# Kernel tuning notes

Measured on AMD Instinct MI355X. Metric: run time of the kernel, lower is better.

The kernel has to match this reference:

```python
import jax, jax.numpy as jnp
import numpy as np

B, S, D, F, E, DT, K = 4, 2048, 1024, 4096, 8, 256, 2


def setup_inputs() -> dict:
    key = jax.random.key(0)
    ks = jax.random.split(key, 8)
    scale_g = 1.0 / np.sqrt(D)
    scale_t = 1.0 / np.sqrt(DT)
    scale_1 = 1.0 / np.sqrt(D)
    scale_2 = 1.0 / np.sqrt(F)
    return {
        "inputs": jax.random.normal(ks[0], (B, S, D), dtype=jnp.float32),
        "task_param": jax.random.normal(ks[1], (B, 1, DT), dtype=jnp.float32),
        "Wg_in": jax.random.normal(ks[2], (D, E), dtype=jnp.float32) * scale_g,
        "bg_in": jnp.zeros((E,), dtype=jnp.float32),
        "Wg_task": jax.random.normal(ks[3], (DT, E), dtype=jnp.float32) * scale_t,
        "bg_task": jnp.zeros((E,), dtype=jnp.float32),
        "alpha": jnp.float32(0.5),
        "W1": jax.random.normal(ks[4], (E, D, F), dtype=jnp.float32) * scale_1,
        "b1": jnp.zeros((E, F), dtype=jnp.float32),
        "W2": jax.random.normal(ks[5], (E, F, D), dtype=jnp.float32) * scale_2,
        "b2": jnp.zeros((E, D), dtype=jnp.float32),
    }


def reference(inputs, task_param, Wg_in, bg_in, Wg_task, bg_task, alpha, W1, b1, W2, b2):
    # Gating: blend input-gate and task-gate logits ([B,1,E] broadcasts over S)
    input_logits = jnp.einsum('bsd,de->bse', inputs, Wg_in) + bg_in
    task_logits = jnp.einsum('btd,de->bte', task_param, Wg_task) + bg_task
    gate_logits = (1.0 - alpha) * input_logits + alpha * task_logits  # [B,S,E]

    topk_vals, selected = jax.lax.top_k(gate_logits, K)  # [B,S,K]

    # Load-balancing auxiliary loss (float32 softmax, as in the original)
    weights_softmax = jax.nn.softmax(gate_logits.astype(jnp.float32), axis=-1).astype(inputs.dtype)
    average_weight = jnp.mean(weights_softmax, axis=(0, 1))  # [E]
    onehot = jax.nn.one_hot(selected, E, dtype=inputs.dtype)  # [B,S,K,E]
    average_count = jnp.mean(onehot.sum(axis=2), axis=(0, 1))  # [E]
    l_aux = jnp.mean(average_weight * average_count) * E

    # Combine weights: softmax over the top-k gate values
    w = jax.nn.softmax(topk_vals.astype(jnp.float32), axis=-1).astype(inputs.dtype)  # [B,S,K]

    # Dense expert compute (same math as the per-expert gather/scatter loop)
    h = jax.nn.silu(jnp.einsum('bsd,edf->ebsf', inputs, W1) + b1[:, None, None, :])  # [E,B,S,F]
    expert_out = jnp.einsum('ebsf,efd->ebsd', h, W2) + b2[:, None, None, :]          # [E,B,S,D]

    picked = jnp.einsum('bske,ebsd->bskd', onehot, expert_out)  # [B,S,K,D]
    results = jnp.einsum('bsk,bskd->bsd', w, picked)            # [B,S,D]
    return results, l_aux.astype(jnp.float32)
```

## Files before the change

### kernel.cpp

```cpp
#include <hip/hip_runtime.h>

#define T_TOK 8192
#define D_DIM 1024
#define F_DIM 4096
#define E_EXP 8
#define DT_DIM 256
#define GBLK 256

#define A_XB   0u
#define A_WT   16777216u
#define A_H    83886080u
#define A_Y    226492416u
#define A_META 262144000u
#define MO_FILL   0
#define MO_PB     64
#define MO_NT     128
#define MO_PARTP  256
#define MO_PARTC  8448
#define MO_TILEE  16640
#define MO_TILERB 17664
#define MO_ROUTEE 18688
#define MO_ROUTEW 84224
#define MO_TSLOT  149760
#define MO_PTOK   215296
#define META_BYTES 284928
#define META_INTS  (META_BYTES/4)

using bf16x8 = __attribute__((ext_vector_type(8))) short;
using f32x4  = __attribute__((ext_vector_type(4))) float;
typedef unsigned short u16;

__device__ __forceinline__ u16 f2bf(float f) {
  union { float f; unsigned u; } v; v.f = f;
  unsigned r = v.u + 0x7FFFu + ((v.u >> 16) & 1u);
  return (u16)(r >> 16);
}
__device__ __forceinline__ float bf2f(u16 h) {
  union { unsigned u; float f; } v; v.u = ((unsigned)h) << 16; return v.f;
}
__device__ __forceinline__ void gload16(const void* gsrc, void* ldst) {
  __builtin_amdgcn_global_load_lds(
      (const __attribute__((address_space(1))) void*)gsrc,
      (__attribute__((address_space(3))) void*)ldst, 16, 0, 0);
}

__global__ void zerok(int* p, int n) {
  int i = blockIdx.x * 256 + threadIdx.x;
  if (i < n) p[i] = 0;
}

__global__ __launch_bounds__(256) void tcvt(const float* __restrict__ src,
                                            u16* __restrict__ dst, int R, int C) {
  __shared__ u16 tile[32][33];
  size_t off = (size_t)blockIdx.z * R * C;
  int cb = blockIdx.x * 32, rb = blockIdx.y * 32;
  int tx = threadIdx.x & 31, ty = threadIdx.x >> 5;
#pragma unroll
  for (int i = 0; i < 4; i++)
    tile[ty + i * 8][tx] = f2bf(src[off + (size_t)(rb + ty + i * 8) * C + cb + tx]);
  __syncthreads();
#pragma unroll
  for (int i = 0; i < 4; i++)
    dst[off + (size_t)(cb + ty + i * 8) * R + rb + tx] = tile[tx][ty + i * 8];
}

__global__ __launch_bounds__(256) void gating(
    const float* __restrict__ X, const float* __restrict__ TP,
    const float* __restrict__ Wg, const float* __restrict__ bg,
    const float* __restrict__ Wt, const float* __restrict__ bgt,
    const float* __restrict__ alphaP, u16* __restrict__ Xb, int* meta) {
  __shared__ float WgT[E_EXP * D_DIM];
  __shared__ float WtT[E_EXP * DT_DIM];
  __shared__ float wsP[4][8];
  __shared__ int   wsC[4][8];
  int tid = threadIdx.x;
  for (int i = tid; i < E_EXP * D_DIM; i += 256) { int d = i >> 3, e = i & 7; WgT[e * D_DIM + d] = Wg[i]; }
  for (int i = tid; i < E_EXP * DT_DIM; i += 256) { int d = i >> 3, e = i & 7; WtT[e * DT_DIM + d] = Wt[i]; }
  __syncthreads();
  int lane = tid & 63, wid = tid >> 6;
  int tb = blockIdx.x * 32;
  int b = tb >> 11;
  float alpha = alphaP[0];

  float tac[8] = {};
#pragma unroll
  for (int i = 0; i < 4; i++) {
    int d = lane + i * 64;
    float x = TP[b * DT_DIM + d];
#pragma unroll
    for (int e = 0; e < 8; e++) tac[e] += x * WtT[e * DT_DIM + d];
  }
  for (int off = 32; off > 0; off >>= 1)
#pragma unroll
    for (int e = 0; e < 8; e++) tac[e] += __shfl_xor(tac[e], off);
  float tl[8];
#pragma unroll
  for (int e = 0; e < 8; e++) tl[e] = alpha * (tac[e] + bgt[e]);

  float psum[8] = {};
  int   cnt[8] = {};
  for (int i = 0; i < 8; i++) {
    int t = tb + wid * 8 + i;
    const float* xr = X + (size_t)t * D_DIM;
    float acc[8] = {};
    u16 xb[16];
#pragma unroll 4
    for (int j = 0; j < 16; j++) {
      int d = lane + j * 64;
      float x = xr[d];
      xb[j] = f2bf(x);
#pragma unroll
      for (int e = 0; e < 8; e++) acc[e] += x * WgT[e * D_DIM + d];
    }
#pragma unroll
    for (int j = 0; j < 16; j++) Xb[(size_t)t * D_DIM + lane + j * 64] = xb[j];
    for (int off = 32; off > 0; off >>= 1)
#pragma unroll
      for (int e = 0; e < 8; e++) acc[e] += __shfl_xor(acc[e], off);
    float gl[8];
#pragma unroll
    for (int e = 0; e < 8; e++) gl[e] = (1.f - alpha) * (acc[e] + bg[e]) + tl[e];
    int e1 = 0;
#pragma unroll
    for (int e = 1; e < 8; e++) if (gl[e] > gl[e1]) e1 = e;
    int es = (e1 == 0) ? 1 : 0;
#pragma unroll
    for (int e = 0; e < 8; e++) if (e != e1 && gl[e] > gl[es]) es = e;
    float mx = gl[0];
#pragma unroll
    for (int e = 1; e < 8; e++) mx = fmaxf(mx, gl[e]);
    float pe[8], se = 0.f;
#pragma unroll
    for (int e = 0; e < 8; e++) { pe[e] = __expf(gl[e] - mx); se += pe[e]; }
    float inv = 1.f / se;
    if (lane == 0) {
#pragma unroll
      for (int e = 0; e < 8; e++) psum[e] += pe[e] * inv;
      cnt[e1]++; cnt[es]++;
      float w1 = 1.f / (1.f + __expf(gl[es] - gl[e1]));
      meta[MO_ROUTEE / 4 + 2 * t] = e1;
      meta[MO_ROUTEE / 4 + 2 * t + 1] = es;
      ((float*)meta)[MO_ROUTEW / 4 + 2 * t] = w1;
      ((float*)meta)[MO_ROUTEW / 4 + 2 * t + 1] = 1.f - w1;
    }
  }
  if (lane == 0) {
#pragma unroll
    for (int e = 0; e < 8; e++) { wsP[wid][e] = psum[e]; wsC[wid][e] = cnt[e]; }
  }
  __syncthreads();
  if (tid < 8) {
    float p = wsP[0][tid] + wsP[1][tid] + wsP[2][tid] + wsP[3][tid];
    int   c = wsC[0][tid] + wsC[1][tid] + wsC[2][tid] + wsC[3][tid];
    ((float*)meta)[MO_PARTP / 4 + blockIdx.x * 8 + tid] = p;
    meta[MO_PARTC / 4 + blockIdx.x * 8 + tid] = c;
  }
}

__global__ void plan(int* meta, float* out) {
  __shared__ float sp[8];
  __shared__ int   sc[8];
  int tid = threadIdx.x;
  if (blockIdx.x != 0) return;
  if (tid < 8) {
    const float* pp = (const float*)meta + MO_PARTP / 4;
    const int*   pc = meta + MO_PARTC / 4;
    float p = 0.f; int c = 0;
    for (int b = 0; b < GBLK; b++) { p += pp[b * 8 + tid]; c += pc[b * 8 + tid]; }
    sp[tid] = p; sc[tid] = c;
  }
  __syncthreads();
  if (tid == 0) {
    int* pb = meta + MO_PB / 4;
    int* tileE = meta + MO_TILEE / 4;
    int* tileRB = meta + MO_TILERB / 4;
    int base = 0, nt = 0;
    float la = 0.f;
    for (int e = 0; e < 8; e++) {
      int n = sc[e];
      pb[e] = base;
      int ntl = (n + 127) >> 7;
      for (int i = 0; i < ntl; i++) { tileE[nt] = e; tileRB[nt] = base + (i << 7); nt++; }
      base += ntl << 7;
      la += (sp[e] * (1.f / 8192.f)) * ((float)n * (1.f / 8192.f));
    }
    pb[8] = base;
    meta[MO_NT / 4] = nt;
    out[T_TOK * D_DIM] = la;
  }
}

__global__ __launch_bounds__(256) void fillk(int* meta) {
  int t = blockIdx.x * 256 + threadIdx.x;
  int lane = threadIdx.x & 63;
  int* pb = meta + MO_PB / 4;
  int* fl = meta + MO_FILL / 4;
  int* ptok = meta + MO_PTOK / 4;
  int* ts = meta + MO_TSLOT / 4;
  unsigned long long lmask = (1ull << lane) - 1;
#pragma unroll
  for (int k = 0; k < 2; k++) {
    int e = meta[MO_ROUTEE / 4 + 2 * t + k];
    int slot = 0;
    for (int ee = 0; ee < 8; ee++) {
      unsigned long long mask = __ballot(e == ee);
      if (e == ee) {
        int low = __ffsll((long long)mask) - 1;
        int pre = __popcll(mask & lmask);
        int base = 0;
        if (lane == low) base = atomicAdd(&fl[ee], __popcll(mask));
        base = __shfl(base, low);
        slot = pb[ee] + base + pre;
      }
    }
    ptok[slot] = t;
    ts[2 * t + k] = slot;
  }
}


__global__ __launch_bounds__(256) void gemm1(
    const u16* __restrict__ Xb, const u16* __restrict__ W1T,
    const float* __restrict__ b1, u16* __restrict__ H, const int* __restrict__ meta) {
  int xcd = blockIdx.x & 7, loc = blockIdx.x >> 3;
  int bt = loc >> 2;
  int cb = (xcd * 4 + (loc & 3)) * 128;
  int nt = meta[MO_NT / 4];
  if (bt >= nt) return;
  int e = meta[MO_TILEE / 4 + bt];
  int rb = meta[MO_TILERB / 4 + bt];
  const int* ptok = meta + MO_PTOK / 4;

  __shared__ short sA[2][128 * 32];
  __shared__ short sB[2][128 * 32];
  int tid = threadIdx.x, lane = tid & 63, wid = tid >> 6;
  int wr = wid >> 1, wc = wid & 1;
  int r0 = tid >> 2;
  int c0 = (((tid & 3) ^ ((r0 >> 1) & 3)) << 3);
  int tok0 = ptok[rb + r0];
  int tok1 = ptok[rb + r0 + 64];
  const u16* gA0 = Xb + (size_t)tok0 * D_DIM + c0;
  const u16* gA1 = Xb + (size_t)tok1 * D_DIM + c0;
  const u16* gB0 = W1T + ((size_t)e * F_DIM + cb + r0) * D_DIM + c0;
  const u16* gB1 = gB0 + (size_t)64 * D_DIM;

#define STAGE_G1(buf, k0)                                              \
  {                                                                    \
    gload16(gA0 + (k0), (char*)&sA[buf][0] + wid * 1024);              \
    gload16(gA1 + (k0), (char*)&sA[buf][0] + 4096 + wid * 1024);       \
    gload16(gB0 + (k0), (char*)&sB[buf][0] + wid * 1024);              \
    gload16(gB1 + (k0), (char*)&sB[buf][0] + 4096 + wid * 1024);       \
  }

  f32x4 acc[4][4] = {};
  int kb = (((lane >> 4) ^ (((lane & 15) >> 1) & 3)) << 3);
  int ra = wr * 64 + (lane & 15);
  int rn = wc * 64 + (lane & 15);
  STAGE_G1(0, 0)
  for (int k0 = 0; k0 < D_DIM; k0 += 32) {
    int c = (k0 >> 5) & 1;
    asm volatile("s_waitcnt vmcnt(0) lgkmcnt(0)" ::: "memory");
    __builtin_amdgcn_sched_barrier(0);
    __builtin_amdgcn_s_barrier();
    if (k0 + 32 < D_DIM) STAGE_G1(c ^ 1, k0 + 32)
    const short* pA = &sA[c][0];
    const short* pB = &sB[c][0];
    bf16x8 af[4], bfr[4];
#pragma unroll
    for (int m = 0; m < 4; m++)
      af[m] = *(const bf16x8*)((const char*)pA + ((ra + m * 16) * 32 + kb) * 2);
#pragma unroll
    for (int n = 0; n < 4; n++)
      bfr[n] = *(const bf16x8*)((const char*)pB + ((rn + n * 16) * 32 + kb) * 2);
    __builtin_amdgcn_s_setprio(1);
#pragma unroll
    for (int m = 0; m < 4; m++)
#pragma unroll
      for (int n = 0; n < 4; n++)
        acc[m][n] = __builtin_amdgcn_mfma_f32_16x16x32_bf16(af[m], bfr[n], acc[m][n], 0, 0, 0);
    __builtin_amdgcn_s_setprio(0);
  }
  int rbase = wr * 64 + ((lane >> 4) << 2);
  int cbase = cb + wc * 64 + (lane & 15);
#pragma unroll
  for (int m = 0; m < 4; m++)
#pragma unroll
    for (int n = 0; n < 4; n++) {
      int f = cbase + n * 16;
      float bias = b1[e * F_DIM + f];
#pragma unroll
      for (int r = 0; r < 4; r++) {
        int p = rb + rbase + m * 16 + r;
        float v = acc[m][n][r] + bias;
        float s = v * (1.0f / (1.0f + __expf(-v)));
        H[(size_t)p * F_DIM + f] = f2bf(s);
      }
    }
}

__global__ __launch_bounds__(256) void gemm2(
    const u16* __restrict__ H, const u16* __restrict__ W2T,
    const float* __restrict__ b2, u16* __restrict__ Y, const int* __restrict__ meta) {
  int id = blockIdx.x;
  int wg = (id & 7) * 136 + (id >> 3);
  int bt = wg >> 3;
  int cb = (wg & 7) * 128;
  int nt = meta[MO_NT / 4];
  if (bt >= nt) return;
  int e = meta[MO_TILEE / 4 + bt];
  int rb = meta[MO_TILERB / 4 + bt];
  __shared__ short sA[2][128 * 32];
  __shared__ short sB[2][128 * 32];
  int tid = threadIdx.x, lane = tid & 63, wid = tid >> 6;
  int wr = wid >> 1, wc = wid & 1;
  int r0 = tid >> 2;
  int c0 = (((tid & 3) ^ ((r0 >> 1) & 3)) << 3);
  const u16* gA0 = H + (size_t)(rb + r0) * F_DIM + c0;
  const u16* gA1 = gA0 + (size_t)64 * F_DIM;
  const u16* gB0 = W2T + ((size_t)e * D_DIM + cb + r0) * F_DIM + c0;
  const u16* gB1 = gB0 + (size_t)64 * F_DIM;

#define STAGE_G2(buf, k0)                                              \
  {                                                                    \
    gload16(gA0 + (k0), (char*)&sA[buf][0] + wid * 1024);              \
    gload16(gA1 + (k0), (char*)&sA[buf][0] + 4096 + wid * 1024);       \
    gload16(gB0 + (k0), (char*)&sB[buf][0] + wid * 1024);              \
    gload16(gB1 + (k0), (char*)&sB[buf][0] + 4096 + wid * 1024);       \
  }

  f32x4 acc[4][4] = {};
  int kb = (((lane >> 4) ^ (((lane & 15) >> 1) & 3)) << 3);
  int ra = wr * 64 + (lane & 15);
  int rn = wc * 64 + (lane & 15);
  STAGE_G2(0, 0)
  for (int k0 = 0; k0 < F_DIM; k0 += 32) {
    int c = (k0 >> 5) & 1;
    asm volatile("s_waitcnt vmcnt(0) lgkmcnt(0)" ::: "memory");
    __builtin_amdgcn_sched_barrier(0);
    __builtin_amdgcn_s_barrier();
    if (k0 + 32 < F_DIM) STAGE_G2(c ^ 1, k0 + 32)
    const short* pA = &sA[c][0];
    const short* pB = &sB[c][0];
    bf16x8 af[4], bfr[4];
#pragma unroll
    for (int m = 0; m < 4; m++)
      af[m] = *(const bf16x8*)((const char*)pA + ((ra + m * 16) * 32 + kb) * 2);
#pragma unroll
    for (int n = 0; n < 4; n++)
      bfr[n] = *(const bf16x8*)((const char*)pB + ((rn + n * 16) * 32 + kb) * 2);
    __builtin_amdgcn_s_setprio(1);
#pragma unroll
    for (int m = 0; m < 4; m++)
#pragma unroll
      for (int n = 0; n < 4; n++)
        acc[m][n] = __builtin_amdgcn_mfma_f32_16x16x32_bf16(af[m], bfr[n], acc[m][n], 0, 0, 0);
    __builtin_amdgcn_s_setprio(0);
  }
  int rbase = wr * 64 + ((lane >> 4) << 2);
  int cbase = cb + wc * 64 + (lane & 15);
#pragma unroll
  for (int m = 0; m < 4; m++)
#pragma unroll
    for (int n = 0; n < 4; n++) {
      int d = cbase + n * 16;
      float bias = b2[e * D_DIM + d];
#pragma unroll
      for (int r = 0; r < 4; r++) {
        int p = rb + rbase + m * 16 + r;
        Y[(size_t)p * D_DIM + d] = f2bf(acc[m][n][r] + bias);
      }
    }
}

__global__ __launch_bounds__(256) void combine(const u16* __restrict__ Y,
                                               const int* __restrict__ meta,
                                               float* __restrict__ out) {
  int t = blockIdx.x;
  const int* ts = meta + MO_TSLOT / 4;
  const float* rw = (const float*)meta + MO_ROUTEW / 4;
  int s1 = ts[2 * t], s2 = ts[2 * t + 1];
  float w1 = rw[2 * t], w2 = rw[2 * t + 1];
  int d0 = threadIdx.x * 4;
  ushort4 a = *(const ushort4*)(Y + (size_t)s1 * D_DIM + d0);
  ushort4 b = *(const ushort4*)(Y + (size_t)s2 * D_DIM + d0);
  float4 v;
  v.x = w1 * bf2f(a.x) + w2 * bf2f(b.x);
  v.y = w1 * bf2f(a.y) + w2 * bf2f(b.y);
  v.z = w1 * bf2f(a.z) + w2 * bf2f(b.z);
  v.w = w1 * bf2f(a.w) + w2 * bf2f(b.w);
  *(float4*)(out + (size_t)t * D_DIM + d0) = v;
}

extern "C" void kernel_launch(void* const* d_in, const int* in_sizes, int n_in,
                              void* d_out, int out_size, void* d_ws, size_t ws_size,
                              hipStream_t stream) {
  (void)in_sizes; (void)n_in; (void)out_size; (void)ws_size;
  const float* X    = (const float*)d_in[0];
  const float* TP   = (const float*)d_in[1];
  const float* Wg   = (const float*)d_in[2];
  const float* bg   = (const float*)d_in[3];
  const float* Wt   = (const float*)d_in[4];
  const float* bgt  = (const float*)d_in[5];
  const float* alp  = (const float*)d_in[6];
  const float* W1   = (const float*)d_in[7];
  const float* b1   = (const float*)d_in[8];
  const float* W2   = (const float*)d_in[9];
  const float* b2   = (const float*)d_in[10];
  float* out = (float*)d_out;
  char* ws = (char*)d_ws;
  u16* Xb = (u16*)(ws + A_XB);
  u16* WT = (u16*)(ws + A_WT);
  u16* H  = (u16*)(ws + A_H);
  u16* Y  = (u16*)(ws + A_Y);
  int* meta = (int*)(ws + A_META);

  zerok<<<(META_INTS + 255) / 256, 256, 0, stream>>>(meta, META_INTS);
  tcvt<<<dim3(F_DIM / 32, D_DIM / 32, E_EXP), 256, 0, stream>>>(W1, WT, D_DIM, F_DIM);
  gating<<<GBLK, 256, 0, stream>>>(X, TP, Wg, bg, Wt, bgt, alp, Xb, meta);
  plan<<<1, 64, 0, stream>>>(meta, out);
  fillk<<<T_TOK / 256, 256, 0, stream>>>(meta);
  gemm1<<<4352, 256, 0, stream>>>(Xb, WT, b1, H, meta);
  tcvt<<<dim3(D_DIM / 32, F_DIM / 32, E_EXP), 256, 0, stream>>>(W2, WT, F_DIM, D_DIM);
  gemm2<<<1088, 256, 0, stream>>>(H, WT, b2, Y, meta);
  combine<<<T_TOK, 256, 0, stream>>>(Y, meta, out);
}
```

Measured before the change: 588.2 us.

## Fuse gating with W1/W2 bf16 transposes into one prep kernel, drop zero kernel

```diff
diff --git a/kernel.cpp b/kernel.cpp
--- a/kernel.cpp
+++ b/kernel.cpp
@@ -12,6 +12,8 @@
 #define A_H    83886080u
 #define A_Y    226492416u
 #define A_META 262144000u
+#define A_W2T  262428928u
+#define W2T_NEED (262428928ull + 67108864ull)
 #define MO_FILL   0
 #define MO_PB     64
 #define MO_NT     128
@@ -24,7 +26,6 @@
 #define MO_TSLOT  149760
 #define MO_PTOK   215296
 #define META_BYTES 284928
-#define META_INTS  (META_BYTES/4)
 
 using bf16x8 = __attribute__((ext_vector_type(8))) short;
 using f32x4  = __attribute__((ext_vector_type(4))) float;
@@ -44,41 +45,66 @@
       (__attribute__((address_space(3))) void*)ldst, 16, 0, 0);
 }
 
-__global__ void zerok(int* p, int n) {
-  int i = blockIdx.x * 256 + threadIdx.x;
-  if (i < n) p[i] = 0;
-}
-
-__global__ __launch_bounds__(256) void tcvt(const float* __restrict__ src,
-                                            u16* __restrict__ dst, int R, int C) {
-  __shared__ u16 tile[32][33];
-  size_t off = (size_t)blockIdx.z * R * C;
-  int cb = blockIdx.x * 32, rb = blockIdx.y * 32;
-  int tx = threadIdx.x & 31, ty = threadIdx.x >> 5;
-#pragma unroll
-  for (int i = 0; i < 4; i++)
-    tile[ty + i * 8][tx] = f2bf(src[off + (size_t)(rb + ty + i * 8) * C + cb + tx]);
+__device__ __forceinline__ void tcvt64_body(const float* __restrict__ src,
+                                            u16* __restrict__ dst, int R, int C,
+                                            int e, int rb, int cb, char* smem) {
+  u16 (*tile)[65] = (u16(*)[65])smem;
+  size_t off = (size_t)e * R * C;
+  int t = threadIdx.x;
+  int r = t >> 4, cq = (t & 15) << 2;
+#pragma unroll
+  for (int k = 0; k < 4; k++) {
+    int rr = r + k * 16;
+    float4 v = *(const float4*)(src + off + (size_t)(rb + rr) * C + cb + cq);
+    tile[rr][cq] = f2bf(v.x);
+    tile[rr][cq + 1] = f2bf(v.y);
+    tile[rr][cq + 2] = f2bf(v.z);
+    tile[rr][cq + 3] = f2bf(v.w);
+  }
   __syncthreads();
-#pragma unroll
-  for (int i = 0; i < 4; i++)
-    dst[off + (size_t)(cb + ty + i * 8) * R + rb + tx] = tile[tx][ty + i * 8];
-}
-
-__global__ __launch_bounds__(256) void gating(
+  int r4 = (t & 15) << 2, c0 = t >> 4;
+#pragma unroll
+  for (int j = 0; j < 4; j++) {
+    int c = c0 + j * 16;
+    ushort4 o;
+    o.x = tile[r4][c]; o.y = tile[r4 + 1][c];
+    o.z = tile[r4 + 2][c]; o.w = tile[r4 + 3][c];
+    *(ushort4*)(dst + off + (size_t)(cb + c) * R + rb + r4) = o;
+  }
+}
+
+__global__ __launch_bounds__(256) void prep(
     const float* __restrict__ X, const float* __restrict__ TP,
     const float* __restrict__ Wg, const float* __restrict__ bg,
     const float* __restrict__ Wt, const float* __restrict__ bgt,
-    const float* __restrict__ alphaP, u16* __restrict__ Xb, int* meta) {
-  __shared__ float WgT[E_EXP * D_DIM];
-  __shared__ float WtT[E_EXP * DT_DIM];
-  __shared__ float wsP[4][8];
-  __shared__ int   wsC[4][8];
+    const float* __restrict__ alphaP,
+    const float* __restrict__ W1, const float* __restrict__ W2,
+    u16* __restrict__ Xb, u16* __restrict__ W1T, u16* __restrict__ W2T,
+    int* meta) {
+  __shared__ char smem[41216];
+  int bid = blockIdx.x;
+  if (bid >= GBLK) {
+    int loc = bid - GBLK;
+    if (loc < 8192) {
+      int e = loc >> 10, t10 = loc & 1023;
+      tcvt64_body(W1, W1T, D_DIM, F_DIM, e, (t10 & 15) << 6, (t10 >> 4) << 6, smem);
+    } else {
+      int l2 = loc - 8192;
+      int e = l2 >> 10, t10 = l2 & 1023;
+      tcvt64_body(W2, W2T, F_DIM, D_DIM, e, (t10 >> 4) << 6, (t10 & 15) << 6, smem);
+    }
+    return;
+  }
+  float* WgT = (float*)smem;
+  float* WtT = (float*)(smem + 32768);
+  float* wsP = (float*)(smem + 40960);
+  int*   wsC = (int*)(smem + 41088);
   int tid = threadIdx.x;
   for (int i = tid; i < E_EXP * D_DIM; i += 256) { int d = i >> 3, e = i & 7; WgT[e * D_DIM + d] = Wg[i]; }
   for (int i = tid; i < E_EXP * DT_DIM; i += 256) { int d = i >> 3, e = i & 7; WtT[e * DT_DIM + d] = Wt[i]; }
   __syncthreads();
   int lane = tid & 63, wid = tid >> 6;
-  int tb = blockIdx.x * 32;
+  int tb = bid * 32;
   int b = tb >> 11;
   float alpha = alphaP[0];
 
@@ -146,15 +172,23 @@
   }
   if (lane == 0) {
 #pragma unroll
-    for (int e = 0; e < 8; e++) { wsP[wid][e] = psum[e]; wsC[wid][e] = cnt[e]; }
+    for (int e = 0; e < 8; e++) { wsP[wid * 8 + e] = psum[e]; wsC[wid * 8 + e] = cnt[e]; }
   }
   __syncthreads();
   if (tid < 8) {
-    float p = wsP[0][tid] + wsP[1][tid] + wsP[2][tid] + wsP[3][tid];
-    int   c = wsC[0][tid] + wsC[1][tid] + wsC[2][tid] + wsC[3][tid];
-    ((float*)meta)[MO_PARTP / 4 + blockIdx.x * 8 + tid] = p;
-    meta[MO_PARTC / 4 + blockIdx.x * 8 + tid] = c;
-  }
+    float p = wsP[tid] + wsP[8 + tid] + wsP[16 + tid] + wsP[24 + tid];
+    int   c = wsC[tid] + wsC[8 + tid] + wsC[16 + tid] + wsC[24 + tid];
+    ((float*)meta)[MO_PARTP / 4 + bid * 8 + tid] = p;
+    meta[MO_PARTC / 4 + bid * 8 + tid] = c;
+  }
+}
+
+__global__ __launch_bounds__(256) void tcvt2k(const float* __restrict__ W2,
+                                              u16* __restrict__ W2T) {
+  __shared__ char smem[8448];
+  int loc = blockIdx.x;
+  int e = loc >> 10, t10 = loc & 1023;
+  tcvt64_body(W2, W2T, F_DIM, D_DIM, e, (t10 >> 4) << 6, (t10 & 15) << 6, smem);
 }
 
 __global__ void plan(int* meta, float* out) {
@@ -168,7 +202,10 @@
     float p = 0.f; int c = 0;
     for (int b = 0; b < GBLK; b++) { p += pp[b * 8 + tid]; c += pc[b * 8 + tid]; }
     sp[tid] = p; sc[tid] = c;
-  }
+    meta[MO_FILL / 4 + tid] = 0;
+  }
+  int* ptok = meta + MO_PTOK / 4;
+  for (int i = tid; i < 17408; i += 64) ptok[i] = 0;
   __syncthreads();
   if (tid == 0) {
     int* pb = meta + MO_PB / 4;
@@ -394,7 +431,7 @@
 extern "C" void kernel_launch(void* const* d_in, const int* in_sizes, int n_in,
                               void* d_out, int out_size, void* d_ws, size_t ws_size,
                               hipStream_t stream) {
-  (void)in_sizes; (void)n_in; (void)out_size; (void)ws_size;
+  (void)in_sizes; (void)n_in; (void)out_size;
   const float* X    = (const float*)d_in[0];
   const float* TP   = (const float*)d_in[1];
   const float* Wg   = (const float*)d_in[2];
@@ -414,13 +451,16 @@
   u16* Y  = (u16*)(ws + A_Y);
   int* meta = (int*)(ws + A_META);
 
-  zerok<<<(META_INTS + 255) / 256, 256, 0, stream>>>(meta, META_INTS);
-  tcvt<<<dim3(F_DIM / 32, D_DIM / 32, E_EXP), 256, 0, stream>>>(W1, WT, D_DIM, F_DIM);
-  gating<<<GBLK, 256, 0, stream>>>(X, TP, Wg, bg, Wt, bgt, alp, Xb, meta);
+  int big = ws_size >= W2T_NEED;
+  u16* W2T = big ? (u16*)(ws + A_W2T) : WT;
+
+  int prep_grid = GBLK + 8192 + (big ? 8192 : 0);
+  prep<<<prep_grid, 256, 0, stream>>>(X, TP, Wg, bg, Wt, bgt, alp, W1, W2,
+                                      Xb, WT, W2T, meta);
   plan<<<1, 64, 0, stream>>>(meta, out);
   fillk<<<T_TOK / 256, 256, 0, stream>>>(meta);
   gemm1<<<4352, 256, 0, stream>>>(Xb, WT, b1, H, meta);
-  tcvt<<<dim3(D_DIM / 32, F_DIM / 32, E_EXP), 256, 0, stream>>>(W2, WT, F_DIM, D_DIM);
-  gemm2<<<1088, 256, 0, stream>>>(H, WT, b2, Y, meta);
+  if (!big) tcvt2k<<<8192, 256, 0, stream>>>(W2, WT);
+  gemm2<<<1088, 256, 0, stream>>>(H, W2T, b2, Y, meta);
   combine<<<T_TOK, 256, 0, stream>>>(Y, meta, out);
 }
```

Result: faster. 567.5 us (-3.5%).
